# Kernel tuning notes

Hardware: AMD Instinct MI355X
Metric: run time of the kernel (lower is better)

## Reference

```python
import jax, jax.numpy as jnp
import numpy as np

N_NODES = 100000
N_EDGES = 3200000
IN_C, HID_C, OUT_C = 128, 16, 5
NEG_SLOPE = 0.2


def setup_inputs() -> dict:
    key = jax.random.key(0)
    ks = jax.random.split(key, 12)
    x = jax.random.normal(ks[0], (N_NODES, IN_C), dtype=jnp.float32)
    edge_index = jax.random.randint(ks[1], (2, N_EDGES), 0, N_NODES, dtype=jnp.int64)
    # GATConv layer 1 params (heads=1)
    s1 = 1.0 / np.sqrt(IN_C)
    W1 = jax.random.uniform(ks[2], (IN_C, HID_C), jnp.float32, -s1, s1)
    att_src1 = jax.random.uniform(ks[3], (HID_C,), jnp.float32, -1.0, 1.0) * s1
    att_dst1 = jax.random.uniform(ks[4], (HID_C,), jnp.float32, -1.0, 1.0) * s1
    b1 = jnp.zeros((HID_C,), jnp.float32)
    # GATConv layer 2 params
    s2 = 1.0 / np.sqrt(HID_C)
    W2 = jax.random.uniform(ks[5], (HID_C, OUT_C), jnp.float32, -s2, s2)
    att_src2 = jax.random.uniform(ks[6], (OUT_C,), jnp.float32, -1.0, 1.0) * s2
    att_dst2 = jax.random.uniform(ks[7], (OUT_C,), jnp.float32, -1.0, 1.0) * s2
    b2 = jnp.zeros((OUT_C,), jnp.float32)
    return {"x": x, "edge_index": edge_index,
            "W1": W1, "att_src1": att_src1, "att_dst1": att_dst1, "b1": b1,
            "W2": W2, "att_src2": att_src2, "att_dst2": att_dst2, "b2": b2}


def gat_layer(x, src, dst, W, att_src, att_dst, bias, n_nodes):
    # project: [N, C_out]
    h = x @ W
    a_src = h @ att_src  # [N]
    a_dst = h @ att_dst  # [N]
    e = a_src[src] + a_dst[dst]            # [E]
    e = jax.nn.leaky_relu(e, NEG_SLOPE)
    # per-destination-node softmax over incoming edges (stable)
    m = jax.ops.segment_max(e, dst, num_segments=n_nodes)
    ex = jnp.exp(e - m[dst])
    denom = jax.ops.segment_sum(ex, dst, num_segments=n_nodes)
    alpha = ex / (denom[dst] + 1e-16)      # [E]
    # weighted scatter-aggregate of source features
    out = jax.ops.segment_sum(h[src] * alpha[:, None], dst, num_segments=n_nodes)
    return out + bias


def reference(x, edge_index, W1, att_src1, att_dst1, b1, W2, att_src2, att_dst2, b2):
    n = x.shape[0]
    loops = jnp.arange(n, dtype=edge_index.dtype)
    src = jnp.concatenate([edge_index[0], loops])  # add_self_loops=True
    dst = jnp.concatenate([edge_index[1], loops])
    h = gat_layer(x, src, dst, W1, att_src1, att_dst1, b1, n)
    h = jax.nn.relu(h)
    h = gat_layer(h, src, dst, W2, att_src2, att_dst2, b2, n)
    return jax.nn.log_softmax(h, axis=1)
```

## Files before the change

kernel.cpp:

```cpp
#include <hip/hip_runtime.h>
#include <hip/hip_fp16.h>

#define N_NODES 100000
#define N_EDGES 3200000
#define E_TOT   (N_EDGES + N_NODES)
#define IN_C 128
#define HID  16
#define OUTC 5
#define NEG_SLOPE 0.2f

#define NBKT 391
#define CAP  9216
#define HCAP 4736
#define P_TILE 8192
#define PART_GRID ((E_TOT + P_TILE - 1) / P_TILE)
#define PROJ_GRID ((N_NODES + 15) / 16)

__device__ __forceinline__ float pk_half2(float a, float b) {
    __half2 h = __halves2half2(__float2half(a), __float2half(b));
    return *(float*)&h;
}
__device__ __forceinline__ float2 unpk_half2(float v) {
    return __half22float2(*(__half2*)&v);
}

__global__ void zero_gcnt_k(int* __restrict__ gcnt) {
    int i = blockIdx.x * blockDim.x + threadIdx.x;
    if (i < NBKT) gcnt[i] = 0;
}

__global__ __launch_bounds__(256) void partproj_k(
    const int* __restrict__ ei, int* __restrict__ gcnt, unsigned* __restrict__ pairs,
    const float* __restrict__ x, const float* __restrict__ W1,
    const float* __restrict__ att_s, const float* __restrict__ att_d,
    __half* __restrict__ h1f, float* __restrict__ a_src, float* __restrict__ a_dst) {
    __shared__ __align__(16) char smem[52288];
    int t = threadIdx.x;
    if (blockIdx.x < PART_GRID) {
        unsigned* vbuf       = (unsigned*)smem;
        unsigned short* bbuf = (unsigned short*)(smem + 32768);
        int* hist            = (int*)(smem + 49152);
        int* cur             = (int*)(smem + 50716);
        for (int i = t; i < NBKT; i += 256) hist[i] = 0;
        __syncthreads();
        int base = blockIdx.x * P_TILE;
        int lim = E_TOT - base; if (lim > P_TILE) lim = P_TILE;
        for (int i = t; i < lim; i += 256) {
            int e = base + i;
            int s, d;
            if (e < N_EDGES) { s = ei[e]; d = ei[N_EDGES + e]; }
            else             { s = e - N_EDGES; d = s; }
            int b = d >> 8;
            vbuf[i] = ((unsigned)s << 8) | (unsigned)(d & 255);
            bbuf[i] = (unsigned short)b;
            atomicAdd(&hist[b], 1);
        }
        __syncthreads();
        for (int i = t; i < NBKT; i += 256) {
            int h = hist[i];
            cur[i] = h ? atomicAdd(&gcnt[i], h) : 0;
        }
        __syncthreads();
        for (int i = t; i < lim; i += 256) {
            int b = bbuf[i];
            int p = atomicAdd(&cur[b], 1);
            if (p >= 0 && p < CAP) pairs[(size_t)b * CAP + p] = vbuf[i];
        }
    } else {
        float* sW = (float*)smem;
        float* sX = (float*)(smem + 8192);
        float* sH = (float*)(smem + 16384);
        int bid = blockIdx.x - PART_GRID;
        const float4* W4 = (const float4*)W1;
        for (int i = t; i < IN_C * HID / 4; i += 256) ((float4*)sW)[i] = W4[i];
        int node0 = bid * 16;
        const float4* x4 = (const float4*)x;
        for (int i = t; i < 16 * IN_C / 4; i += 256) {
            int r = i >> 5, c4 = i & 31;
            int node = node0 + r;
            float4 v = make_float4(0.f, 0.f, 0.f, 0.f);
            if (node < N_NODES) v = x4[(size_t)node * 32 + c4];
            *((float4*)&sX[r * IN_C + c4 * 4]) = v;
        }
        __syncthreads();
        int r = t >> 4, c = t & 15;
        int node = node0 + r;
        float acc = 0.0f;
        #pragma unroll 8
        for (int k = 0; k < IN_C; ++k) acc += sX[r * IN_C + k] * sW[k * HID + c];
        sH[r * HID + c] = acc;
        if (node < N_NODES) h1f[(size_t)node * HID + c] = __float2half(acc);
        __syncthreads();
        if (c == 0 && node < N_NODES) {
            float s = 0.0f, d = 0.0f;
            #pragma unroll
            for (int k = 0; k < HID; ++k) {
                float hv = sH[r * HID + k];
                s += hv * att_s[k];
                d += hv * att_d[k];
            }
            a_src[node] = s;
            a_dst[node] = d;
        }
    }
}

__global__ __launch_bounds__(256) void gat1s_k(
    const unsigned* __restrict__ pairs, const int* __restrict__ gcnt,
    const __half* __restrict__ h1f, const float* __restrict__ asrc1,
    const float* __restrict__ adst1, const float* __restrict__ b1,
    const float* __restrict__ W2, const float* __restrict__ as2,
    const float* __restrict__ ad2, float4* __restrict__ h2p,
    float* __restrict__ adst2) {
    __shared__ int ccnt[128], sexc[128], cur[128];
    __shared__ int lcsr[HCAP];
    __shared__ float adt[128];
    __shared__ float sW2[HID * OUTC];
    __shared__ float sB1[HID];
    __shared__ float sAs[OUTC], sAd[OUTC];
    int t = threadIdx.x;
    int parent = blockIdx.x >> 1, half = blockIdx.x & 1;
    if (t < 128) ccnt[t] = 0;
    else {
        int idx = t - 128;
        int node = (parent << 8) + (half << 7) + idx;
        adt[idx] = (node < N_NODES) ? adst1[node] : 0.0f;
    }
    if (t < HID * OUTC) sW2[t] = W2[t];
    if (t < HID) sB1[t] = b1[t];
    if (t < OUTC) { sAs[t] = as2[t]; sAd[t] = ad2[t]; }
    __syncthreads();
    int tot = gcnt[parent]; if (tot > CAP) tot = CAP; if (tot < 0) tot = 0;
    size_t pb = (size_t)parent * CAP;
    for (int i = t; i < tot; i += 256) {
        unsigned v = pairs[pb + i];
        int dl = (int)(v & 255u);
        if ((dl >> 7) == half) atomicAdd(&ccnt[dl & 127], 1);
    }
    __syncthreads();
    if (t < 128) sexc[t] = ccnt[t];
    __syncthreads();
    for (int off = 1; off < 128; off <<= 1) {
        int xv = 0;
        if (t < 128 && t >= off) xv = sexc[t - off];
        __syncthreads();
        if (t < 128) sexc[t] += xv;
        __syncthreads();
    }
    if (t < 128) { int e = sexc[t] - ccnt[t]; sexc[t] = e; cur[t] = e; }
    __syncthreads();
    for (int i = t; i < tot; i += 256) {
        unsigned v = pairs[pb + i];
        int dl = (int)(v & 255u);
        if ((dl >> 7) == half) {
            int pos = atomicAdd(&cur[dl & 127], 1);
            if (pos < HCAP) lcsr[pos] = (int)(v >> 8);
        }
    }
    __syncthreads();
    int g = t >> 4, lane = t & 15;
    for (int batch = 0; batch < 8; ++batch) {
        int nl = batch * 16 + g;
        int node = (parent << 8) + (half << 7) + nl;
        int start = sexc[nl];
        int len = ccnt[nl];
        if (start > HCAP) start = HCAP;
        if (start + len > HCAP) len = HCAP - start;
        float ad = adt[nl];
        float acc[HID];
        #pragma unroll
        for (int c = 0; c < HID; ++c) acc[c] = 0.0f;
        float accd = 0.0f;
        for (int it = lane; it < len; it += 16) {
            int s = lcsr[start + it];
            float v = asrc1[s] + ad;
            v = (v > 0.0f) ? v : NEG_SLOPE * v;
            float ex = __expf(v);
            accd += ex;
            const float4* hp = (const float4*)(h1f + (size_t)s * HID);
            float4 r0 = hp[0], r1 = hp[1];
            float2 f0 = unpk_half2(r0.x), f1 = unpk_half2(r0.y);
            float2 f2 = unpk_half2(r0.z), f3 = unpk_half2(r0.w);
            float2 f4 = unpk_half2(r1.x), f5 = unpk_half2(r1.y);
            float2 f6 = unpk_half2(r1.z), f7 = unpk_half2(r1.w);
            acc[0]  += ex * f0.x; acc[1]  += ex * f0.y;
            acc[2]  += ex * f1.x; acc[3]  += ex * f1.y;
            acc[4]  += ex * f2.x; acc[5]  += ex * f2.y;
            acc[6]  += ex * f3.x; acc[7]  += ex * f3.y;
            acc[8]  += ex * f4.x; acc[9]  += ex * f4.y;
            acc[10] += ex * f5.x; acc[11] += ex * f5.y;
            acc[12] += ex * f6.x; acc[13] += ex * f6.y;
            acc[14] += ex * f7.x; acc[15] += ex * f7.y;
        }
        #pragma unroll
        for (int off = 8; off; off >>= 1) {
            accd += __shfl_xor(accd, off);
            #pragma unroll
            for (int c = 0; c < HID; ++c) acc[c] += __shfl_xor(acc[c], off);
        }
        if (lane == 0 && node < N_NODES) {
            float inv = 1.0f / (accd + 1e-16f);
            float gg[HID];
            #pragma unroll
            for (int k = 0; k < HID; ++k) gg[k] = fmaxf(acc[k] * inv + sB1[k], 0.0f);
            float h2[OUTC];
            #pragma unroll
            for (int c = 0; c < OUTC; ++c) {
                float a = 0.0f;
                #pragma unroll
                for (int k = 0; k < HID; ++k) a += gg[k] * sW2[k * OUTC + c];
                h2[c] = a;
            }
            float s2 = 0.0f, d2 = 0.0f;
            #pragma unroll
            for (int c = 0; c < OUTC; ++c) { s2 += h2[c] * sAs[c]; d2 += h2[c] * sAd[c]; }
            adst2[node] = d2;
            float4 r;
            r.x = s2;
            r.y = pk_half2(h2[0], h2[1]);
            r.z = pk_half2(h2[2], h2[3]);
            r.w = pk_half2(h2[4], 0.0f);
            h2p[node] = r;
        }
    }
}

__global__ __launch_bounds__(256) void gat2s_k(
    const unsigned* __restrict__ pairs, const int* __restrict__ gcnt,
    const float4* __restrict__ h2p, const float* __restrict__ adst2,
    const float* __restrict__ b2, float* __restrict__ out) {
    __shared__ int ccnt[128], sexc[128], cur[128];
    __shared__ int lcsr[HCAP];
    __shared__ float adt[128];
    __shared__ float sB2[OUTC];
    int t = threadIdx.x;
    int parent = blockIdx.x >> 1, half = blockIdx.x & 1;
    if (t < 128) ccnt[t] = 0;
    else {
        int idx = t - 128;
        int node = (parent << 8) + (half << 7) + idx;
        adt[idx] = (node < N_NODES) ? adst2[node] : 0.0f;
    }
    if (t < OUTC) sB2[t] = b2[t];
    __syncthreads();
    int tot = gcnt[parent]; if (tot > CAP) tot = CAP; if (tot < 0) tot = 0;
    size_t pb = (size_t)parent * CAP;
    for (int i = t; i < tot; i += 256) {
        unsigned v = pairs[pb + i];
        int dl = (int)(v & 255u);
        if ((dl >> 7) == half) atomicAdd(&ccnt[dl & 127], 1);
    }
    __syncthreads();
    if (t < 128) sexc[t] = ccnt[t];
    __syncthreads();
    for (int off = 1; off < 128; off <<= 1) {
        int xv = 0;
        if (t < 128 && t >= off) xv = sexc[t - off];
        __syncthreads();
        if (t < 128) sexc[t] += xv;
        __syncthreads();
    }
    if (t < 128) { int e = sexc[t] - ccnt[t]; sexc[t] = e; cur[t] = e; }
    __syncthreads();
    for (int i = t; i < tot; i += 256) {
        unsigned v = pairs[pb + i];
        int dl = (int)(v & 255u);
        if ((dl >> 7) == half) {
            int pos = atomicAdd(&cur[dl & 127], 1);
            if (pos < HCAP) lcsr[pos] = (int)(v >> 8);
        }
    }
    __syncthreads();
    int g = t >> 4, lane = t & 15;
    for (int batch = 0; batch < 8; ++batch) {
        int nl = batch * 16 + g;
        int node = (parent << 8) + (half << 7) + nl;
        int start = sexc[nl];
        int len = ccnt[nl];
        if (start > HCAP) start = HCAP;
        if (start + len > HCAP) len = HCAP - start;
        float ad = adt[nl];
        float acc[OUTC];
        #pragma unroll
        for (int c = 0; c < OUTC; ++c) acc[c] = 0.0f;
        float accd = 0.0f;
        for (int it = lane; it < len; it += 16) {
            int s = lcsr[start + it];
            float4 r = h2p[s];
            float v = r.x + ad;
            v = (v > 0.0f) ? v : NEG_SLOPE * v;
            float ex = __expf(v);
            accd += ex;
            float2 f01 = unpk_half2(r.y);
            float2 f23 = unpk_half2(r.z);
            float2 f4_ = unpk_half2(r.w);
            acc[0] += ex * f01.x; acc[1] += ex * f01.y;
            acc[2] += ex * f23.x; acc[3] += ex * f23.y;
            acc[4] += ex * f4_.x;
        }
        #pragma unroll
        for (int off = 8; off; off >>= 1) {
            accd += __shfl_xor(accd, off);
            #pragma unroll
            for (int c = 0; c < OUTC; ++c) acc[c] += __shfl_xor(acc[c], off);
        }
        if (lane == 0 && node < N_NODES) {
            float inv = 1.0f / (accd + 1e-16f);
            float val[OUTC];
            float mx = -3.4e38f;
            #pragma unroll
            for (int c = 0; c < OUTC; ++c) {
                val[c] = acc[c] * inv + sB2[c];
                mx = fmaxf(mx, val[c]);
            }
            float se = 0.0f;
            #pragma unroll
            for (int c = 0; c < OUTC; ++c) se += __expf(val[c] - mx);
            float lse = logf(se) + mx;
            #pragma unroll
            for (int c = 0; c < OUTC; ++c)
                out[(size_t)node * OUTC + c] = val[c] - lse;
        }
    }
}

extern "C" void kernel_launch(void* const* d_in, const int* in_sizes, int n_in,
                              void* d_out, int out_size, void* d_ws, size_t ws_size,
                              hipStream_t stream) {
    const float* x    = (const float*)d_in[0];
    const int*   ei   = (const int*)d_in[1];
    const float* W1   = (const float*)d_in[2];
    const float* as1  = (const float*)d_in[3];
    const float* ad1  = (const float*)d_in[4];
    const float* b1   = (const float*)d_in[5];
    const float* W2   = (const float*)d_in[6];
    const float* as2  = (const float*)d_in[7];
    const float* ad2  = (const float*)d_in[8];
    const float* b2   = (const float*)d_in[9];
    float* out = (float*)d_out;

    char* wsb = (char*)d_ws;
    unsigned* pairs = (unsigned*)wsb;
    float4* h2p     = (float4*)(wsb + (size_t)NBKT * CAP * 4);
    __half* h1f     = (__half*)((char*)h2p + (size_t)N_NODES * 16);
    float*  asrc1   = (float*)((char*)h1f + (size_t)N_NODES * HID * 2);
    float*  adst1   = asrc1 + N_NODES;
    float*  adst2   = adst1 + N_NODES;
    int*    gcnt    = (int*)(adst2 + N_NODES);

    zero_gcnt_k<<<(NBKT + 255) / 256, 256, 0, stream>>>(gcnt);
    partproj_k<<<PART_GRID + PROJ_GRID, 256, 0, stream>>>(
        ei, gcnt, pairs, x, W1, as1, ad1, h1f, asrc1, adst1);
    gat1s_k<<<NBKT * 2, 256, 0, stream>>>(pairs, gcnt, h1f, asrc1, adst1, b1,
                                          W2, as2, ad2, h2p, adst2);
    gat2s_k<<<NBKT * 2, 256, 0, stream>>>(pairs, gcnt, h2p, adst2, b2, out);
}
```

Baseline: 276.1 us.

## Build global CSR once and share it across both GAT aggregation kernels

Adds a separate build kernel that turns the bucketed (src,dst) pairs into a global CSR with per-node start/count, instead of each GAT kernel rebuilding a shared-memory CSR from the pairs. The two aggregation kernels become lightweight one-node-per-16-lanes kernels with a 2x-unrolled edge loop, cutting the duplicated counting, scan and scatter work and the large LDS footprint. The cost is an extra kernel launch plus a global CSR write and read-back. The zero kernel is also replaced by hipMemsetAsync.

```diff
diff --git a/kernel.cpp b/kernel.cpp
--- a/kernel.cpp
+++ b/kernel.cpp
@@ -11,7 +11,7 @@
 
 #define NBKT 391
 #define CAP  9216
-#define HCAP 4736
+#define HALF_CAP 4608
 #define P_TILE 8192
 #define PART_GRID ((E_TOT + P_TILE - 1) / P_TILE)
 #define PROJ_GRID ((N_NODES + 15) / 16)
@@ -22,11 +22,6 @@
 }
 __device__ __forceinline__ float2 unpk_half2(float v) {
     return __half22float2(*(__half2*)&v);
-}
-
-__global__ void zero_gcnt_k(int* __restrict__ gcnt) {
-    int i = blockIdx.x * blockDim.x + threadIdx.x;
-    if (i < NBKT) gcnt[i] = 0;
 }
 
 __global__ __launch_bounds__(256) void partproj_k(
@@ -105,222 +100,252 @@
     }
 }
 
-__global__ __launch_bounds__(256) void gat1s_k(
-    const unsigned* __restrict__ pairs, const int* __restrict__ gcnt,
+__global__ __launch_bounds__(256) void build_k(const unsigned* __restrict__ pairs,
+                                               const int* __restrict__ gcnt,
+                                               int* __restrict__ csr,
+                                               int2* __restrict__ rs_cnt) {
+    __shared__ int ccnt[128], sexc[128], cur[128];
+    int t = threadIdx.x;
+    int parent = blockIdx.x >> 1, half = blockIdx.x & 1;
+    if (t < 128) ccnt[t] = 0;
+    __syncthreads();
+    int tot = gcnt[parent];
+    if (tot > CAP) tot = CAP; if (tot < 0) tot = 0;
+    size_t pb = (size_t)parent * CAP;
+    for (int i = t; i < tot; i += 256) {
+        unsigned v = pairs[pb + i];
+        int dl = (int)(v & 255u);
+        if ((dl >> 7) == half) atomicAdd(&ccnt[dl & 127], 1);
+    }
+    __syncthreads();
+    if (t < 128) sexc[t] = ccnt[t];
+    __syncthreads();
+    for (int off = 1; off < 128; off <<= 1) {
+        int xv = 0;
+        if (t < 128 && t >= off) xv = sexc[t - off];
+        __syncthreads();
+        if (t < 128) sexc[t] += xv;
+        __syncthreads();
+    }
+    int gbase = (int)pb + half * HALF_CAP;
+    int regend = gbase + HALF_CAP;
+    if (t < 128) {
+        int excl = sexc[t] - ccnt[t];
+        sexc[t] = excl;
+        cur[t] = gbase + excl;
+        int node = (parent << 8) + (half << 7) + t;
+        if (node < N_NODES) {
+            int c = ccnt[t];
+            if (excl + c > HALF_CAP) c = (excl < HALF_CAP) ? (HALF_CAP - excl) : 0;
+            rs_cnt[node] = make_int2(gbase + excl, c);
+        }
+    }
+    __syncthreads();
+    for (int i = t; i < tot; i += 256) {
+        unsigned v = pairs[pb + i];
+        int dl = (int)(v & 255u);
+        if ((dl >> 7) == half) {
+            int pos = atomicAdd(&cur[dl & 127], 1);
+            if (pos < regend) csr[pos] = (int)(v >> 8);
+        }
+    }
+}
+
+__global__ __launch_bounds__(256) void gat1_k(
+    const int* __restrict__ csr, const int2* __restrict__ rs_cnt,
     const __half* __restrict__ h1f, const float* __restrict__ asrc1,
     const float* __restrict__ adst1, const float* __restrict__ b1,
     const float* __restrict__ W2, const float* __restrict__ as2,
     const float* __restrict__ ad2, float4* __restrict__ h2p,
     float* __restrict__ adst2) {
-    __shared__ int ccnt[128], sexc[128], cur[128];
-    __shared__ int lcsr[HCAP];
-    __shared__ float adt[128];
     __shared__ float sW2[HID * OUTC];
     __shared__ float sB1[HID];
     __shared__ float sAs[OUTC], sAd[OUTC];
     int t = threadIdx.x;
-    int parent = blockIdx.x >> 1, half = blockIdx.x & 1;
-    if (t < 128) ccnt[t] = 0;
-    else {
-        int idx = t - 128;
-        int node = (parent << 8) + (half << 7) + idx;
-        adt[idx] = (node < N_NODES) ? adst1[node] : 0.0f;
-    }
     if (t < HID * OUTC) sW2[t] = W2[t];
     if (t < HID) sB1[t] = b1[t];
     if (t < OUTC) { sAs[t] = as2[t]; sAd[t] = ad2[t]; }
     __syncthreads();
-    int tot = gcnt[parent]; if (tot > CAP) tot = CAP; if (tot < 0) tot = 0;
-    size_t pb = (size_t)parent * CAP;
-    for (int i = t; i < tot; i += 256) {
-        unsigned v = pairs[pb + i];
-        int dl = (int)(v & 255u);
-        if ((dl >> 7) == half) atomicAdd(&ccnt[dl & 127], 1);
-    }
-    __syncthreads();
-    if (t < 128) sexc[t] = ccnt[t];
-    __syncthreads();
-    for (int off = 1; off < 128; off <<= 1) {
-        int xv = 0;
-        if (t < 128 && t >= off) xv = sexc[t - off];
-        __syncthreads();
-        if (t < 128) sexc[t] += xv;
-        __syncthreads();
-    }
-    if (t < 128) { int e = sexc[t] - ccnt[t]; sexc[t] = e; cur[t] = e; }
-    __syncthreads();
-    for (int i = t; i < tot; i += 256) {
-        unsigned v = pairs[pb + i];
-        int dl = (int)(v & 255u);
-        if ((dl >> 7) == half) {
-            int pos = atomicAdd(&cur[dl & 127], 1);
-            if (pos < HCAP) lcsr[pos] = (int)(v >> 8);
-        }
-    }
-    __syncthreads();
-    int g = t >> 4, lane = t & 15;
-    for (int batch = 0; batch < 8; ++batch) {
-        int nl = batch * 16 + g;
-        int node = (parent << 8) + (half << 7) + nl;
-        int start = sexc[nl];
-        int len = ccnt[nl];
-        if (start > HCAP) start = HCAP;
-        if (start + len > HCAP) len = HCAP - start;
-        float ad = adt[nl];
-        float acc[HID];
-        #pragma unroll
-        for (int c = 0; c < HID; ++c) acc[c] = 0.0f;
-        float accd = 0.0f;
-        for (int it = lane; it < len; it += 16) {
-            int s = lcsr[start + it];
-            float v = asrc1[s] + ad;
-            v = (v > 0.0f) ? v : NEG_SLOPE * v;
-            float ex = __expf(v);
-            accd += ex;
-            const float4* hp = (const float4*)(h1f + (size_t)s * HID);
-            float4 r0 = hp[0], r1 = hp[1];
-            float2 f0 = unpk_half2(r0.x), f1 = unpk_half2(r0.y);
-            float2 f2 = unpk_half2(r0.z), f3 = unpk_half2(r0.w);
-            float2 f4 = unpk_half2(r1.x), f5 = unpk_half2(r1.y);
-            float2 f6 = unpk_half2(r1.z), f7 = unpk_half2(r1.w);
-            acc[0]  += ex * f0.x; acc[1]  += ex * f0.y;
-            acc[2]  += ex * f1.x; acc[3]  += ex * f1.y;
-            acc[4]  += ex * f2.x; acc[5]  += ex * f2.y;
-            acc[6]  += ex * f3.x; acc[7]  += ex * f3.y;
-            acc[8]  += ex * f4.x; acc[9]  += ex * f4.y;
-            acc[10] += ex * f5.x; acc[11] += ex * f5.y;
-            acc[12] += ex * f6.x; acc[13] += ex * f6.y;
-            acc[14] += ex * f7.x; acc[15] += ex * f7.y;
-        }
-        #pragma unroll
-        for (int off = 8; off; off >>= 1) {
-            accd += __shfl_xor(accd, off);
+
+    int node = (blockIdx.x * 256 + t) >> 4;
+    int lane = t & 15;
+    int2 rc = rs_cnt[node];
+    int start = rc.x, len = rc.y;
+    float ad  = adst1[node];
+
+    float acc[HID];
+    #pragma unroll
+    for (int c = 0; c < HID; ++c) acc[c] = 0.0f;
+    float accd = 0.0f;
+    int it = lane;
+    for (; it + 16 < len; it += 32) {
+        int s0 = csr[start + it];
+        int s1 = csr[start + it + 16];
+        float v0 = asrc1[s0] + ad;
+        float v1 = asrc1[s1] + ad;
+        const float4* hp0 = (const float4*)(h1f + (size_t)s0 * HID);
+        const float4* hp1 = (const float4*)(h1f + (size_t)s1 * HID);
+        float4 p0 = hp0[0], p1 = hp0[1];
+        float4 q0 = hp1[0], q1 = hp1[1];
+        v0 = (v0 > 0.0f) ? v0 : NEG_SLOPE * v0;
+        v1 = (v1 > 0.0f) ? v1 : NEG_SLOPE * v1;
+        float e0 = __expf(v0), e1 = __expf(v1);
+        accd += e0 + e1;
+        {
+            float2 f0 = unpk_half2(p0.x), f1 = unpk_half2(p0.y);
+            float2 f2 = unpk_half2(p0.z), f3 = unpk_half2(p0.w);
+            float2 f4 = unpk_half2(p1.x), f5 = unpk_half2(p1.y);
+            float2 f6 = unpk_half2(p1.z), f7 = unpk_half2(p1.w);
+            acc[0]  += e0 * f0.x; acc[1]  += e0 * f0.y;
+            acc[2]  += e0 * f1.x; acc[3]  += e0 * f1.y;
+            acc[4]  += e0 * f2.x; acc[5]  += e0 * f2.y;
+            acc[6]  += e0 * f3.x; acc[7]  += e0 * f3.y;
+            acc[8]  += e0 * f4.x; acc[9]  += e0 * f4.y;
+            acc[10] += e0 * f5.x; acc[11] += e0 * f5.y;
+            acc[12] += e0 * f6.x; acc[13] += e0 * f6.y;
+            acc[14] += e0 * f7.x; acc[15] += e0 * f7.y;
+        }
+        {
+            float2 f0 = unpk_half2(q0.x), f1 = unpk_half2(q0.y);
+            float2 f2 = unpk_half2(q0.z), f3 = unpk_half2(q0.w);
+            float2 f4 = unpk_half2(q1.x), f5 = unpk_half2(q1.y);
+            float2 f6 = unpk_half2(q1.z), f7 = unpk_half2(q1.w);
+            acc[0]  += e1 * f0.x; acc[1]  += e1 * f0.y;
+            acc[2]  += e1 * f1.x; acc[3]  += e1 * f1.y;
+            acc[4]  += e1 * f2.x; acc[5]  += e1 * f2.y;
+            acc[6]  += e1 * f3.x; acc[7]  += e1 * f3.y;
+            acc[8]  += e1 * f4.x; acc[9]  += e1 * f4.y;
+            acc[10] += e1 * f5.x; acc[11] += e1 * f5.y;
+            acc[12] += e1 * f6.x; acc[13] += e1 * f6.y;
+            acc[14] += e1 * f7.x; acc[15] += e1 * f7.y;
+        }
+    }
+    if (it < len) {
+        int s = csr[start + it];
+        float v = asrc1[s] + ad;
+        v = (v > 0.0f) ? v : NEG_SLOPE * v;
+        float ex = __expf(v);
+        accd += ex;
+        const float4* hp = (const float4*)(h1f + (size_t)s * HID);
+        float4 r0 = hp[0], r1 = hp[1];
+        float2 f0 = unpk_half2(r0.x), f1 = unpk_half2(r0.y);
+        float2 f2 = unpk_half2(r0.z), f3 = unpk_half2(r0.w);
+        float2 f4 = unpk_half2(r1.x), f5 = unpk_half2(r1.y);
+        float2 f6 = unpk_half2(r1.z), f7 = unpk_half2(r1.w);
+        acc[0]  += ex * f0.x; acc[1]  += ex * f0.y;
+        acc[2]  += ex * f1.x; acc[3]  += ex * f1.y;
+        acc[4]  += ex * f2.x; acc[5]  += ex * f2.y;
+        acc[6]  += ex * f3.x; acc[7]  += ex * f3.y;
+        acc[8]  += ex * f4.x; acc[9]  += ex * f4.y;
+        acc[10] += ex * f5.x; acc[11] += ex * f5.y;
+        acc[12] += ex * f6.x; acc[13] += ex * f6.y;
+        acc[14] += ex * f7.x; acc[15] += ex * f7.y;
+    }
+    #pragma unroll
+    for (int off = 8; off; off >>= 1) {
+        accd += __shfl_xor(accd, off);
+        #pragma unroll
+        for (int c = 0; c < HID; ++c) acc[c] += __shfl_xor(acc[c], off);
+    }
+    if (lane == 0) {
+        float inv = 1.0f / (accd + 1e-16f);
+        float g[HID];
+        #pragma unroll
+        for (int k = 0; k < HID; ++k) g[k] = fmaxf(acc[k] * inv + sB1[k], 0.0f);
+        float h2[OUTC];
+        #pragma unroll
+        for (int c = 0; c < OUTC; ++c) {
+            float a = 0.0f;
             #pragma unroll
-            for (int c = 0; c < HID; ++c) acc[c] += __shfl_xor(acc[c], off);
-        }
-        if (lane == 0 && node < N_NODES) {
-            float inv = 1.0f / (accd + 1e-16f);
-            float gg[HID];
-            #pragma unroll
-            for (int k = 0; k < HID; ++k) gg[k] = fmaxf(acc[k] * inv + sB1[k], 0.0f);
-            float h2[OUTC];
-            #pragma unroll
-            for (int c = 0; c < OUTC; ++c) {
-                float a = 0.0f;
-                #pragma unroll
-                for (int k = 0; k < HID; ++k) a += gg[k] * sW2[k * OUTC + c];
-                h2[c] = a;
-            }
-            float s2 = 0.0f, d2 = 0.0f;
-            #pragma unroll
-            for (int c = 0; c < OUTC; ++c) { s2 += h2[c] * sAs[c]; d2 += h2[c] * sAd[c]; }
-            adst2[node] = d2;
-            float4 r;
-            r.x = s2;
-            r.y = pk_half2(h2[0], h2[1]);
-            r.z = pk_half2(h2[2], h2[3]);
-            r.w = pk_half2(h2[4], 0.0f);
-            h2p[node] = r;
-        }
-    }
-}
-
-__global__ __launch_bounds__(256) void gat2s_k(
-    const unsigned* __restrict__ pairs, const int* __restrict__ gcnt,
+            for (int k = 0; k < HID; ++k) a += g[k] * sW2[k * OUTC + c];
+            h2[c] = a;
+        }
+        float s2 = 0.0f, d2 = 0.0f;
+        #pragma unroll
+        for (int c = 0; c < OUTC; ++c) { s2 += h2[c] * sAs[c]; d2 += h2[c] * sAd[c]; }
+        adst2[node] = d2;
+        float4 r;
+        r.x = s2;
+        r.y = pk_half2(h2[0], h2[1]);
+        r.z = pk_half2(h2[2], h2[3]);
+        r.w = pk_half2(h2[4], 0.0f);
+        h2p[node] = r;
+    }
+}
+
+__global__ __launch_bounds__(256) void gat2_k(
+    const int* __restrict__ csr, const int2* __restrict__ rs_cnt,
     const float4* __restrict__ h2p, const float* __restrict__ adst2,
     const float* __restrict__ b2, float* __restrict__ out) {
-    __shared__ int ccnt[128], sexc[128], cur[128];
-    __shared__ int lcsr[HCAP];
-    __shared__ float adt[128];
     __shared__ float sB2[OUTC];
     int t = threadIdx.x;
-    int parent = blockIdx.x >> 1, half = blockIdx.x & 1;
-    if (t < 128) ccnt[t] = 0;
-    else {
-        int idx = t - 128;
-        int node = (parent << 8) + (half << 7) + idx;
-        adt[idx] = (node < N_NODES) ? adst2[node] : 0.0f;
-    }
     if (t < OUTC) sB2[t] = b2[t];
     __syncthreads();
-    int tot = gcnt[parent]; if (tot > CAP) tot = CAP; if (tot < 0) tot = 0;
-    size_t pb = (size_t)parent * CAP;
-    for (int i = t; i < tot; i += 256) {
-        unsigned v = pairs[pb + i];
-        int dl = (int)(v & 255u);
-        if ((dl >> 7) == half) atomicAdd(&ccnt[dl & 127], 1);
-    }
-    __syncthreads();
-    if (t < 128) sexc[t] = ccnt[t];
-    __syncthreads();
-    for (int off = 1; off < 128; off <<= 1) {
-        int xv = 0;
-        if (t < 128 && t >= off) xv = sexc[t - off];
-        __syncthreads();
-        if (t < 128) sexc[t] += xv;
-        __syncthreads();
-    }
-    if (t < 128) { int e = sexc[t] - ccnt[t]; sexc[t] = e; cur[t] = e; }
-    __syncthreads();
-    for (int i = t; i < tot; i += 256) {
-        unsigned v = pairs[pb + i];
-        int dl = (int)(v & 255u);
-        if ((dl >> 7) == half) {
-            int pos = atomicAdd(&cur[dl & 127], 1);
-            if (pos < HCAP) lcsr[pos] = (int)(v >> 8);
-        }
-    }
-    __syncthreads();
-    int g = t >> 4, lane = t & 15;
-    for (int batch = 0; batch < 8; ++batch) {
-        int nl = batch * 16 + g;
-        int node = (parent << 8) + (half << 7) + nl;
-        int start = sexc[nl];
-        int len = ccnt[nl];
-        if (start > HCAP) start = HCAP;
-        if (start + len > HCAP) len = HCAP - start;
-        float ad = adt[nl];
-        float acc[OUTC];
-        #pragma unroll
-        for (int c = 0; c < OUTC; ++c) acc[c] = 0.0f;
-        float accd = 0.0f;
-        for (int it = lane; it < len; it += 16) {
-            int s = lcsr[start + it];
-            float4 r = h2p[s];
-            float v = r.x + ad;
-            v = (v > 0.0f) ? v : NEG_SLOPE * v;
-            float ex = __expf(v);
-            accd += ex;
-            float2 f01 = unpk_half2(r.y);
-            float2 f23 = unpk_half2(r.z);
-            float2 f4_ = unpk_half2(r.w);
-            acc[0] += ex * f01.x; acc[1] += ex * f01.y;
-            acc[2] += ex * f23.x; acc[3] += ex * f23.y;
-            acc[4] += ex * f4_.x;
-        }
-        #pragma unroll
-        for (int off = 8; off; off >>= 1) {
-            accd += __shfl_xor(accd, off);
-            #pragma unroll
-            for (int c = 0; c < OUTC; ++c) acc[c] += __shfl_xor(acc[c], off);
-        }
-        if (lane == 0 && node < N_NODES) {
-            float inv = 1.0f / (accd + 1e-16f);
-            float val[OUTC];
-            float mx = -3.4e38f;
-            #pragma unroll
-            for (int c = 0; c < OUTC; ++c) {
-                val[c] = acc[c] * inv + sB2[c];
-                mx = fmaxf(mx, val[c]);
-            }
-            float se = 0.0f;
-            #pragma unroll
-            for (int c = 0; c < OUTC; ++c) se += __expf(val[c] - mx);
-            float lse = logf(se) + mx;
-            #pragma unroll
-            for (int c = 0; c < OUTC; ++c)
-                out[(size_t)node * OUTC + c] = val[c] - lse;
-        }
+
+    int node = (blockIdx.x * 256 + t) >> 4;
+    int lane = t & 15;
+    int2 rc = rs_cnt[node];
+    int start = rc.x, len = rc.y;
+    float ad  = adst2[node];
+
+    float acc[OUTC];
+    #pragma unroll
+    for (int c = 0; c < OUTC; ++c) acc[c] = 0.0f;
+    float accd = 0.0f;
+    int it = lane;
+    for (; it + 16 < len; it += 32) {
+        int s0 = csr[start + it];
+        int s1 = csr[start + it + 16];
+        float4 r0 = h2p[s0];
+        float4 r1 = h2p[s1];
+        float v0 = r0.x + ad;
+        float v1 = r1.x + ad;
+        v0 = (v0 > 0.0f) ? v0 : NEG_SLOPE * v0;
+        v1 = (v1 > 0.0f) ? v1 : NEG_SLOPE * v1;
+        float e0 = __expf(v0), e1 = __expf(v1);
+        accd += e0 + e1;
+        float2 a01 = unpk_half2(r0.y), a23 = unpk_half2(r0.z), a4 = unpk_half2(r0.w);
+        float2 b01 = unpk_half2(r1.y), b23 = unpk_half2(r1.z), b4 = unpk_half2(r1.w);
+        acc[0] += e0 * a01.x + e1 * b01.x;
+        acc[1] += e0 * a01.y + e1 * b01.y;
+        acc[2] += e0 * a23.x + e1 * b23.x;
+        acc[3] += e0 * a23.y + e1 * b23.y;
+        acc[4] += e0 * a4.x  + e1 * b4.x;
+    }
+    if (it < len) {
+        int s = csr[start + it];
+        float4 r = h2p[s];
+        float v = r.x + ad;
+        v = (v > 0.0f) ? v : NEG_SLOPE * v;
+        float ex = __expf(v);
+        accd += ex;
+        float2 f01 = unpk_half2(r.y), f23 = unpk_half2(r.z), f4 = unpk_half2(r.w);
+        acc[0] += ex * f01.x; acc[1] += ex * f01.y;
+        acc[2] += ex * f23.x; acc[3] += ex * f23.y;
+        acc[4] += ex * f4.x;
+    }
+    #pragma unroll
+    for (int off = 8; off; off >>= 1) {
+        accd += __shfl_xor(accd, off);
+        #pragma unroll
+        for (int c = 0; c < OUTC; ++c) acc[c] += __shfl_xor(acc[c], off);
+    }
+    if (lane == 0) {
+        float inv = 1.0f / (accd + 1e-16f);
+        float val[OUTC];
+        float mx = -3.4e38f;
+        #pragma unroll
+        for (int c = 0; c < OUTC; ++c) {
+            val[c] = acc[c] * inv + sB2[c];
+            mx = fmaxf(mx, val[c]);
+        }
+        float se = 0.0f;
+        #pragma unroll
+        for (int c = 0; c < OUTC; ++c) se += __expf(val[c] - mx);
+        float lse = logf(se) + mx;
+        #pragma unroll
+        for (int c = 0; c < OUTC; ++c)
+            out[(size_t)node * OUTC + c] = val[c] - lse;
     }
 }
 
@@ -341,17 +366,20 @@
 
     char* wsb = (char*)d_ws;
     unsigned* pairs = (unsigned*)wsb;
-    float4* h2p     = (float4*)(wsb + (size_t)NBKT * CAP * 4);
-    __half* h1f     = (__half*)((char*)h2p + (size_t)N_NODES * 16);
-    float*  asrc1   = (float*)((char*)h1f + (size_t)N_NODES * HID * 2);
-    float*  adst1   = asrc1 + N_NODES;
-    float*  adst2   = adst1 + N_NODES;
-    int*    gcnt    = (int*)(adst2 + N_NODES);
-
-    zero_gcnt_k<<<(NBKT + 255) / 256, 256, 0, stream>>>(gcnt);
+    float4* h2p     = (float4*)wsb;
+    float*  adst2   = (float*)(wsb + 1600000);
+    int*    csr     = (int*)(wsb + 14413824);
+    __half* h1f     = (__half*)(wsb + 28827648);
+    float*  asrc1   = (float*)(wsb + 32027648);
+    float*  adst1   = (float*)(wsb + 32427648);
+    int2*   rs_cnt  = (int2*)(wsb + 32827648);
+    int*    gcnt    = (int*)(wsb + 33627648);
+
+    hipMemsetAsync(gcnt, 0, NBKT * sizeof(int), stream);
     partproj_k<<<PART_GRID + PROJ_GRID, 256, 0, stream>>>(
         ei, gcnt, pairs, x, W1, as1, ad1, h1f, asrc1, adst1);
-    gat1s_k<<<NBKT * 2, 256, 0, stream>>>(pairs, gcnt, h1f, asrc1, adst1, b1,
+    build_k<<<NBKT * 2, 256, 0, stream>>>(pairs, gcnt, csr, rs_cnt);
+    gat1_k<<<PROJ_GRID, 256, 0, stream>>>(csr, rs_cnt, h1f, asrc1, adst1, b1,
                                           W2, as2, ad2, h2p, adst2);
-    gat2s_k<<<NBKT * 2, 256, 0, stream>>>(pairs, gcnt, h2p, adst2, b2, out);
-}
+    gat2_k<<<PROJ_GRID, 256, 0, stream>>>(csr, rs_cnt, h2p, adst2, b2, out);
+}
```

Measured after the change: 253.1 us. 1.09x faster.
